# Kernel optimization log

Measured on AMD Instinct MI355X. Metric: run time of the kernel, lower is better.

The kernel has to match this reference:

```python
import jax, jax.numpy as jnp
import numpy as np

CODEBOOK_SIZE = 1024
EMBEDDING_DIM = 256
COMMITMENT_COST = 0.25


def setup_inputs() -> dict:
    key = jax.random.key(0)
    k1, k2 = jax.random.split(key)
    x = jax.random.normal(k1, (32, EMBEDDING_DIM, 32, 32), dtype=jnp.float32)
    # embedding initialized uniform(-1/K, 1/K) like the torch module
    embedding = jax.random.uniform(
        k2, (CODEBOOK_SIZE, EMBEDDING_DIM), dtype=jnp.float32,
        minval=-1.0 / CODEBOOK_SIZE, maxval=1.0 / CODEBOOK_SIZE)
    return {"x": x, "embedding": embedding}


def reference(x, embedding):
    # x: [B, C, H, W] -> inputs: [B, H, W, C]
    inputs = jnp.transpose(x, (0, 2, 3, 1))
    input_shape = inputs.shape
    flat = inputs.reshape(-1, EMBEDDING_DIM)  # [N, D]
    # squared L2 distances to codebook: [N, K]
    distances = (jnp.sum(flat ** 2, axis=1, keepdims=True)
                 + jnp.sum(embedding ** 2, axis=1)
                 - 2.0 * flat @ embedding.T)
    encoding_indices = jnp.argmin(distances, axis=1)  # [N]
    encodings = jax.nn.one_hot(encoding_indices, CODEBOOK_SIZE, dtype=jnp.float32)  # [N, K]
    # gather (same math as encodings @ embedding)
    quantized = embedding[encoding_indices].reshape(input_shape)  # [B, H, W, C]
    e_latent_loss = jnp.mean((jax.lax.stop_gradient(quantized) - inputs) ** 2)
    q_latent_loss = jnp.mean((quantized - jax.lax.stop_gradient(inputs)) ** 2)
    loss = q_latent_loss + COMMITMENT_COST * e_latent_loss
    # straight-through estimator
    quantized_st = inputs + jax.lax.stop_gradient(quantized - inputs)
    return (loss, jnp.transpose(quantized_st, (0, 3, 1, 2)), encodings)
```

## Files before the change

### kernel.cpp

```cpp
#include <hip/hip_runtime.h>
#include <cstdint>
#include <cstddef>

constexpr int B = 32, C = 256, H = 32, W = 32;
constexpr int NPTS = B * H * W;
constexpr int DIM  = 256;
constexpr int K    = 1024;
constexpr int QELEMS = B * C * H * W;
constexpr int CHW = C * H * W;

typedef __attribute__((ext_vector_type(8))) short s8v;
typedef __attribute__((ext_vector_type(4))) float f32x4;

#define GLD_LDS16(g, l)                                                        \
  __builtin_amdgcn_global_load_lds(                                            \
      (const __attribute__((address_space(1))) unsigned int*)(g),              \
      (__attribute__((address_space(3))) unsigned int*)(l), 16, 0, 0)

__device__ __forceinline__ unsigned short f2bf(float f) {
  unsigned u = __float_as_uint(f);
  return (unsigned short)((u + 0x7FFFu + ((u >> 16) & 1u)) >> 16);
}

__global__ __launch_bounds__(256) void prep_kernel(
    const float* __restrict__ x, const float* __restrict__ emb,
    unsigned short* __restrict__ ehi, float* __restrict__ esq,
    unsigned short* __restrict__ xhi, float* __restrict__ xsq) {
  __shared__ float xls[DIM][32];
  const int t = threadIdx.x;
  const int bid = blockIdx.x;

  if (bid < 16) {
    float (*sums)[64] = (float (*)[64])xls;
    const int k = bid * 64 + (t & 63);
    const int seg = t >> 6;
    const float* er = emb + (size_t)k * DIM + seg * 64;
    float v[64];
    float4* v4 = (float4*)v;
#pragma unroll
    for (int i = 0; i < 16; ++i) v4[i] = *(const float4*)(er + i * 4);
    float s = 0.f;
#pragma unroll
    for (int i = 0; i < 64; ++i) s = fmaf(v[i], v[i], s);
    unsigned short* eo = ehi + (size_t)k * DIM + seg * 64;
#pragma unroll
    for (int i = 0; i < 8; ++i) {
      unsigned short h[8];
#pragma unroll
      for (int j = 0; j < 8; ++j) h[j] = f2bf(v[i * 8 + j]);
      *(s8v*)(eo + i * 8) = *(s8v*)h;
    }
    sums[seg][t & 63] = s;
    __syncthreads();
    if (t < 64)
      esq[bid * 64 + t] =
          ((sums[0][t] + sums[1][t]) + sums[2][t]) + sums[3][t];
    return;
  }

  const int n0 = (bid - 16) * 32;
  const int bb = n0 >> 10, hw0 = n0 & 1023;
  const float* xb = x + (size_t)bb * CHW + hw0;
  const int lane = t & 63, w = t >> 6;
  const int row_off = lane >> 3;
  const int p4 = (lane & 7) * 4;
#pragma unroll
  for (int i = 0; i < 8; ++i) {
    const int c0 = w * 64 + i * 8;
    GLD_LDS16(xb + (size_t)(c0 + row_off) * 1024 + p4, &xls[c0][0]);
  }
  __syncthreads();

  if (t < 32) {
    float s = 0.f;
#pragma unroll 8
    for (int c = 0; c < 256; ++c) {
      const float v = xls[c][t];
      s = fmaf(v, v, s);
    }
    xsq[n0 + t] = s;
  }
  const int p2 = t & 31, cb = (t >> 5) * 32;
  unsigned short* xo = xhi + (size_t)(n0 + p2) * DIM + cb;
#pragma unroll
  for (int i = 0; i < 4; ++i) {
    unsigned short h[8];
#pragma unroll
    for (int j = 0; j < 8; ++j) h[j] = f2bf(xls[cb + i * 8 + j][p2]);
    *(s8v*)(xo + i * 8) = *(s8v*)h;
  }
}

constexpr float MARGIN = 1e-3f;
__global__ __launch_bounds__(256) void coarse_kernel(
    const unsigned short* __restrict__ xhi, const unsigned short* __restrict__ ehi,
    const float* __restrict__ esq, const float* __restrict__ xsq,
    float* __restrict__ part, unsigned int* __restrict__ cand) {
  __shared__ __align__(16) unsigned short xs[128][32];
  __shared__ __align__(16) unsigned short es[128][32];
  __shared__ float xsq_s[128], esq_s[128], thr_s[128];
  __shared__ unsigned long long red2[2][128];
  __shared__ unsigned int cntL[128];

  const int t = threadIdx.x;
  const int lane = t & 63, w = t >> 6;
  const int wn = (w & 1) * 64, wk = (w >> 1) * 64;
  const int col = lane & 15, quad = lane >> 4;
  const int nblk = blockIdx.x * 128;
  const int kblk = blockIdx.y * 128;

  if (t < 128) {
    xsq_s[t] = xsq[nblk + t];
    esq_s[t] = esq[kblk + t];
    cntL[t] = 0u;
  }

  f32x4 acc[4][4];
#pragma unroll
  for (int i = 0; i < 4; ++i)
#pragma unroll
    for (int j = 0; j < 4; ++j) acc[i][j] = (f32x4){0.f, 0.f, 0.f, 0.f};

  const int gl_row = lane >> 2;
  const int gl_c   = (lane & 3) * 8;

  for (int c0 = 0; c0 < DIM; c0 += 32) {
    __syncthreads();
#pragma unroll
    for (int i = 0; i < 2; ++i) {
      const int inst = w + 4 * i;
      const int row = inst * 16 + gl_row;
      GLD_LDS16(xhi + (size_t)(nblk + row) * DIM + c0 + gl_c, &xs[inst * 16][0]);
      GLD_LDS16(ehi + (size_t)(kblk + row) * DIM + c0 + gl_c, &es[inst * 16][0]);
    }
    __syncthreads();
    s8v a[4], b[4];
#pragma unroll
    for (int ti = 0; ti < 4; ++ti)
      a[ti] = *(const s8v*)&xs[wn + ti * 16 + col][quad * 8];
#pragma unroll
    for (int tj = 0; tj < 4; ++tj)
      b[tj] = *(const s8v*)&es[wk + tj * 16 + col][quad * 8];
#pragma unroll
    for (int ti = 0; ti < 4; ++ti)
#pragma unroll
      for (int tj = 0; tj < 4; ++tj)
        acc[ti][tj] = __builtin_amdgcn_mfma_f32_16x16x32_bf16(
            a[ti], b[tj], acc[ti][tj], 0, 0, 0);
  }

  unsigned long long nmin[4][4];
#pragma unroll
  for (int ti = 0; ti < 4; ++ti)
#pragma unroll
    for (int r = 0; r < 4; ++r) nmin[ti][r] = ~0ULL;
#pragma unroll
  for (int ti = 0; ti < 4; ++ti)
#pragma unroll
    for (int tj = 0; tj < 4; ++tj) {
      const int krel = wk + tj * 16 + col;
      const float eq = esq_s[krel];
#pragma unroll
      for (int r = 0; r < 4; ++r) {
        const int nl = wn + ti * 16 + quad * 4 + r;
        const float d = (xsq_s[nl] + eq) - 2.f * acc[ti][tj][r];
        const unsigned long long key =
            ((unsigned long long)__float_as_uint(d) << 32) |
            (unsigned)(kblk + krel);
        if (key < nmin[ti][r]) nmin[ti][r] = key;
      }
    }
#pragma unroll
  for (int o = 1; o < 16; o <<= 1)
#pragma unroll
    for (int ti = 0; ti < 4; ++ti)
#pragma unroll
      for (int r = 0; r < 4; ++r) {
        const unsigned long long v = __shfl_xor(nmin[ti][r], o, 64);
        if (v < nmin[ti][r]) nmin[ti][r] = v;
      }
  if (col == 0) {
#pragma unroll
    for (int ti = 0; ti < 4; ++ti)
#pragma unroll
      for (int r = 0; r < 4; ++r)
        red2[w >> 1][wn + ti * 16 + quad * 4 + r] = nmin[ti][r];
  }
  __syncthreads();
  if (t < 128) {
    const unsigned long long m0 = red2[0][t], m1 = red2[1][t];
    const unsigned long long m = (m1 < m0) ? m1 : m0;
    const float dmin = __uint_as_float((unsigned)(m >> 32));
    part[(size_t)(nblk + t) * 8 + blockIdx.y] = dmin;
    thr_s[t] = dmin + MARGIN;
  }
  __syncthreads();
#pragma unroll
  for (int ti = 0; ti < 4; ++ti)
#pragma unroll
    for (int tj = 0; tj < 4; ++tj) {
      const int krel = wk + tj * 16 + col;
      const float eq = esq_s[krel];
#pragma unroll
      for (int r = 0; r < 4; ++r) {
        const int nl = wn + ti * 16 + quad * 4 + r;
        const float d = (xsq_s[nl] + eq) - 2.f * acc[ti][tj][r];
        if (d <= thr_s[nl]) {
          const unsigned slot = atomicAdd(&cntL[nl], 1u);
          if (slot < 4u)
            cand[((size_t)(nblk + nl) * 8 + blockIdx.y) * 4 + slot] =
                (unsigned)(kblk + krel);
        }
      }
    }
  __syncthreads();
  if (t < 128) {
    unsigned c = cntL[t];
    const size_t base = ((size_t)(nblk + t) * 8 + blockIdx.y) * 4;
    if (c > 4u) { cand[base + 3] = 0xFFFFFFFEu; c = 3u; }
    for (unsigned s = c; s < 4u; ++s) cand[base + s] = 0xFFFFFFFFu;
  }
}

__global__ __launch_bounds__(256) void resolve_kernel(
    const float* __restrict__ x, const float* __restrict__ emb,
    const float* __restrict__ esq, const float* __restrict__ xsq,
    const float* __restrict__ part, const unsigned int* __restrict__ cand,
    int* __restrict__ ids_g) {
  __shared__ __align__(16) float xls[DIM][17];
  __shared__ unsigned list[512];
  __shared__ unsigned long long best[16];
  __shared__ float thr_s[16];
  __shared__ float xsq_s[16];
  __shared__ int lcnt;

  const int t = threadIdx.x;
  const int n0 = blockIdx.x * 16;
  const int bb = n0 >> 10, hw0 = n0 & 1023;

  const float* xb = x + (size_t)bb * CHW + hw0;
  {
    const int p = t & 15, cs = t >> 4;
#pragma unroll 4
    for (int r = 0; r < 16; ++r) {
      const int c = r * 16 + cs;
      xls[c][p] = xb[(size_t)c * 1024 + p];
    }
  }
  if (t == 0) lcnt = 0;
  if (t < 16) {
    best[t] = ~0ULL;
    xsq_s[t] = xsq[n0 + t];
    const float4 p0 = *(const float4*)&part[(size_t)(n0 + t) * 8];
    const float4 p1 = *(const float4*)&part[(size_t)(n0 + t) * 8 + 4];
    float g = fminf(fminf(fminf(p0.x, p0.y), fminf(p0.z, p0.w)),
                    fminf(fminf(p1.x, p1.y), fminf(p1.z, p1.w)));
    thr_s[t] = g + MARGIN;
  }
  __syncthreads();

  if (t < 128) {
    const int nn = t >> 3, s = t & 7;
    const float pv = part[(size_t)(n0 + nn) * 8 + s];
    if (pv <= thr_s[nn]) {
      const uint4 c4 = *(const uint4*)&cand[((size_t)(n0 + nn) * 8 + s) * 4];
      const unsigned vs[4] = {c4.x, c4.y, c4.z, c4.w};
#pragma unroll
      for (int i = 0; i < 4; ++i) {
        const unsigned v = vs[i];
        if (v == 0xFFFFFFFFu) continue;
        const unsigned entry = (v == 0xFFFFFFFEu)
                                   ? ((unsigned)nn << 11) | 1024u | (unsigned)s
                                   : ((unsigned)nn << 11) | (v & 1023u);
        const int pos = atomicAdd(&lcnt, 1);
        if (pos < 512) list[pos] = entry;
      }
    }
  }
  __syncthreads();

  const int L = lcnt < 512 ? lcnt : 512;
  for (int e = t; e < L; e += 256) {
    const unsigned entry = list[e];
    const int p = entry >> 11;
    const float xq = xsq_s[p];
    int klo, khi;
    if (entry & 1024u) { const int s = entry & 7; klo = s * 128; khi = klo + 128; }
    else               { klo = entry & 1023u; khi = klo + 1; }
    for (int k = klo; k < khi; ++k) {
      const float* er = emb + (size_t)k * DIM;
      float dot = 0.f;
#pragma unroll 4
      for (int c4 = 0; c4 < DIM; c4 += 4) {
        const float4 e4 = *(const float4*)(er + c4);
        dot = fmaf(xls[c4 + 0][p], e4.x, dot);
        dot = fmaf(xls[c4 + 1][p], e4.y, dot);
        dot = fmaf(xls[c4 + 2][p], e4.z, dot);
        dot = fmaf(xls[c4 + 3][p], e4.w, dot);
      }
      const float t1 = xq + esq[k];
      const float d = t1 - 2.f * dot;
      const unsigned long long key =
          ((unsigned long long)__float_as_uint(d) << 32) | (unsigned)k;
      atomicMin(&best[p], key);
    }
  }
  __syncthreads();
  if (t < 16) ids_g[n0 + t] = (int)(best[t] & 0xFFFFFFFFu);
}

__global__ __launch_bounds__(256) void enc_kernel(
    const int* __restrict__ ids_g, float* __restrict__ enc) {
  __shared__ int ids_s[16];
  const int t = threadIdx.x;
  const int n0 = blockIdx.x * 16;
  if (t < 16) ids_s[t] = ids_g[n0 + t];
  __syncthreads();

  float* sl = enc + (size_t)blockIdx.x * 16384;
  float4* b4 = (float4*)(sl + 3);
#pragma unroll
  for (int j = 0; j < 16; ++j) {
    const int idx = t + j * 256;
    if (idx < 4095) {
      const int lf = 3 + 4 * idx;
      float4 v;
      v.x = (((lf + 0) & 1023) == ids_s[(lf + 0) >> 10]) ? 1.f : 0.f;
      v.y = (((lf + 1) & 1023) == ids_s[(lf + 1) >> 10]) ? 1.f : 0.f;
      v.z = (((lf + 2) & 1023) == ids_s[(lf + 2) >> 10]) ? 1.f : 0.f;
      v.w = (((lf + 3) & 1023) == ids_s[(lf + 3) >> 10]) ? 1.f : 0.f;
      b4[idx] = v;
    }
  }
  if (t == 0) {
    sl[0] = (ids_s[0] == 0) ? 1.f : 0.f;
    sl[1] = (ids_s[0] == 1) ? 1.f : 0.f;
    sl[2] = (ids_s[0] == 2) ? 1.f : 0.f;
    sl[16383] = (ids_s[15] == 1023) ? 1.f : 0.f;
  }
}

__global__ __launch_bounds__(256) void outq_kernel(
    const float* __restrict__ x, const float* __restrict__ emb,
    const int* __restrict__ ids_g, float* __restrict__ outq,
    float* __restrict__ lws) {
  __shared__ int ids_s[1024];
  __shared__ float lred[4];
  const int t = threadIdx.x;
  const int bb = blockIdx.x >> 5;
  const int c0 = (blockIdx.x & 31) * 8;

#pragma unroll
  for (int i = 0; i < 4; ++i) ids_s[t + i * 256] = ids_g[bb * 1024 + t + i * 256];
  __syncthreads();

  const float* xb = x + (size_t)bb * CHW;
  float* ob = outq + (size_t)bb * CHW;
  float lsum = 0.f;
#pragma unroll
  for (int i = 0; i < 4; ++i) {
    const int hw = t + i * 256;
    const int id = ids_s[hw];
    const float* er = emb + (size_t)id * DIM + c0;
    const float4 e0 = *(const float4*)(er);
    const float4 e1 = *(const float4*)(er + 4);
    const float q[8] = {e0.x, e0.y, e0.z, e0.w, e1.x, e1.y, e1.z, e1.w};
#pragma unroll
    for (int ci = 0; ci < 8; ++ci) {
      const float xv = xb[(size_t)(c0 + ci) * 1024 + hw];
      ob[(size_t)(c0 + ci) * 1024 + hw] = q[ci];
      const float d = q[ci] - xv;
      lsum = fmaf(d, d, lsum);
    }
  }

  float s = lsum;
#pragma unroll
  for (int o = 32; o > 0; o >>= 1) s += __shfl_down(s, o, 64);
  if ((t & 63) == 0) lred[t >> 6] = s;
  __syncthreads();
  if (t == 0)
    lws[blockIdx.x] = ((lred[0] + lred[1]) + lred[2]) + lred[3];
}

__global__ __launch_bounds__(256) void loss_reduce(
    const float* __restrict__ lws, float* __restrict__ loss) {
  __shared__ float red[4];
  const int t = threadIdx.x;
  float s = 0.f;
#pragma unroll
  for (int i = 0; i < 4; ++i) s += lws[t + i * 256];
#pragma unroll
  for (int o = 32; o > 0; o >>= 1) s += __shfl_down(s, o, 64);
  if ((t & 63) == 0) red[t >> 6] = s;
  __syncthreads();
  if (t == 0)
    *loss = (((red[0] + red[1]) + red[2]) + red[3]) * (1.25f / (float)QELEMS);
}

extern "C" void kernel_launch(void* const* d_in, const int* in_sizes, int n_in,
                              void* d_out, int out_size, void* d_ws, size_t ws_size,
                              hipStream_t stream) {
  const float* x   = (const float*)d_in[0];
  const float* emb = (const float*)d_in[1];
  float* out  = (float*)d_out;
  float* loss = out;
  float* outq = out + 1;
  float* enc  = out + 1 + QELEMS;

  char* ws = (char*)d_ws;
  unsigned short* ehi  = (unsigned short*)ws;
  float*          esq  = (float*)(ws + 524288);
  float*          xsq  = (float*)(ws + 528384);
  float*          part = (float*)(ws + 659456);
  unsigned int*   cand = (unsigned int*)(ws + 1708032);
  unsigned short* xhi  = (unsigned short*)(ws + 5902336);
  float*          lws  = (float*)(ws + 22679552);
  int*            ids  = (int*)(ws + 22683648);

  prep_kernel<<<16 + 1024, 256, 0, stream>>>(x, emb, ehi, esq, xhi, xsq);
  dim3 cg(NPTS / 128, 8);
  coarse_kernel<<<cg, 256, 0, stream>>>(xhi, ehi, esq, xsq, part, cand);
  resolve_kernel<<<NPTS / 16, 256, 0, stream>>>(x, emb, esq, xsq, part, cand,
                                                ids);
  enc_kernel<<<NPTS / 16, 256, 0, stream>>>(ids, enc);
  outq_kernel<<<1024, 256, 0, stream>>>(x, emb, ids, outq, lws);
  loss_reduce<<<1, 256, 0, stream>>>(lws, loss);
}
```

Baseline: 293.2 us.

## Fuse one-hot and quantized output kernels and derive loss from min distances

The resolve kernel now handles 32 points per block and computes each block's loss partial by summing the winning squared distances. This removes the need to re-read x in a separate loss pass. The one-hot encoding writer and the quantized-output gather are merged into one kernel, and both use nontemporal stores. The aim is to save the extra full read of x plus one kernel launch, at the cost of computing the loss from the expanded-distance formula, which can lose some precision to cancellation.

```diff
diff --git a/kernel.cpp b/kernel.cpp
--- a/kernel.cpp
+++ b/kernel.cpp
@@ -20,6 +20,13 @@
 __device__ __forceinline__ unsigned short f2bf(float f) {
   unsigned u = __float_as_uint(f);
   return (unsigned short)((u + 0x7FFFu + ((u >> 16) & 1u)) >> 16);
+}
+
+__device__ __forceinline__ void nt_store4(float* p, f32x4 v) {
+  __builtin_nontemporal_store(v, (f32x4*)p);
+}
+__device__ __forceinline__ void nt_store1(float* p, float v) {
+  __builtin_nontemporal_store(v, p);
 }
 
 __global__ __launch_bounds__(256) void prep_kernel(
@@ -226,29 +233,29 @@
     const float* __restrict__ x, const float* __restrict__ emb,
     const float* __restrict__ esq, const float* __restrict__ xsq,
     const float* __restrict__ part, const unsigned int* __restrict__ cand,
-    int* __restrict__ ids_g) {
-  __shared__ __align__(16) float xls[DIM][17];
-  __shared__ unsigned list[512];
-  __shared__ unsigned long long best[16];
-  __shared__ float thr_s[16];
-  __shared__ float xsq_s[16];
+    int* __restrict__ ids_g, float* __restrict__ lws) {
+  __shared__ __align__(16) float xls[DIM][33];
+  __shared__ unsigned list[1024];
+  __shared__ unsigned long long best[32];
+  __shared__ float thr_s[32];
+  __shared__ float xsq_s[32];
   __shared__ int lcnt;
 
   const int t = threadIdx.x;
-  const int n0 = blockIdx.x * 16;
+  const int n0 = blockIdx.x * 32;
   const int bb = n0 >> 10, hw0 = n0 & 1023;
 
   const float* xb = x + (size_t)bb * CHW + hw0;
   {
-    const int p = t & 15, cs = t >> 4;
-#pragma unroll 4
-    for (int r = 0; r < 16; ++r) {
-      const int c = r * 16 + cs;
+    const int p = t & 31, cs = t >> 5;
+#pragma unroll 8
+    for (int r = 0; r < 32; ++r) {
+      const int c = r * 8 + cs;
       xls[c][p] = xb[(size_t)c * 1024 + p];
     }
   }
   if (t == 0) lcnt = 0;
-  if (t < 16) {
+  if (t < 32) {
     best[t] = ~0ULL;
     xsq_s[t] = xsq[n0 + t];
     const float4 p0 = *(const float4*)&part[(size_t)(n0 + t) * 8];
@@ -259,7 +266,7 @@
   }
   __syncthreads();
 
-  if (t < 128) {
+  {
     const int nn = t >> 3, s = t & 7;
     const float pv = part[(size_t)(n0 + nn) * 8 + s];
     if (pv <= thr_s[nn]) {
@@ -273,13 +280,13 @@
                                    ? ((unsigned)nn << 11) | 1024u | (unsigned)s
                                    : ((unsigned)nn << 11) | (v & 1023u);
         const int pos = atomicAdd(&lcnt, 1);
-        if (pos < 512) list[pos] = entry;
-      }
-    }
-  }
-  __syncthreads();
-
-  const int L = lcnt < 512 ? lcnt : 512;
+        if (pos < 1024) list[pos] = entry;
+      }
+    }
+  }
+  __syncthreads();
+
+  const int L = lcnt < 1024 ? lcnt : 1024;
   for (int e = t; e < L; e += 256) {
     const unsigned entry = list[e];
     const int p = entry >> 11;
@@ -306,81 +313,64 @@
     }
   }
   __syncthreads();
-  if (t < 16) ids_g[n0 + t] = (int)(best[t] & 0xFFFFFFFFu);
-}
-
-__global__ __launch_bounds__(256) void enc_kernel(
-    const int* __restrict__ ids_g, float* __restrict__ enc) {
-  __shared__ int ids_s[16];
+  if (t < 32) {
+    ids_g[n0 + t] = (int)(best[t] & 0xFFFFFFFFu);
+    float s = __uint_as_float((unsigned)(best[t] >> 32));
+#pragma unroll
+    for (int o = 16; o > 0; o >>= 1) s += __shfl_down(s, o, 64);
+    if (t == 0) lws[blockIdx.x] = s;
+  }
+}
+
+__global__ __launch_bounds__(256) void encq_kernel(
+    const float* __restrict__ emb, const int* __restrict__ ids_g,
+    float* __restrict__ enc, float* __restrict__ outq) {
+  __shared__ int ids_s[32];
   const int t = threadIdx.x;
-  const int n0 = blockIdx.x * 16;
-  if (t < 16) ids_s[t] = ids_g[n0 + t];
-  __syncthreads();
-
-  float* sl = enc + (size_t)blockIdx.x * 16384;
-  float4* b4 = (float4*)(sl + 3);
-#pragma unroll
-  for (int j = 0; j < 16; ++j) {
-    const int idx = t + j * 256;
-    if (idx < 4095) {
-      const int lf = 3 + 4 * idx;
-      float4 v;
-      v.x = (((lf + 0) & 1023) == ids_s[(lf + 0) >> 10]) ? 1.f : 0.f;
-      v.y = (((lf + 1) & 1023) == ids_s[(lf + 1) >> 10]) ? 1.f : 0.f;
-      v.z = (((lf + 2) & 1023) == ids_s[(lf + 2) >> 10]) ? 1.f : 0.f;
-      v.w = (((lf + 3) & 1023) == ids_s[(lf + 3) >> 10]) ? 1.f : 0.f;
-      b4[idx] = v;
-    }
-  }
-  if (t == 0) {
-    sl[0] = (ids_s[0] == 0) ? 1.f : 0.f;
-    sl[1] = (ids_s[0] == 1) ? 1.f : 0.f;
-    sl[2] = (ids_s[0] == 2) ? 1.f : 0.f;
-    sl[16383] = (ids_s[15] == 1023) ? 1.f : 0.f;
-  }
-}
-
-__global__ __launch_bounds__(256) void outq_kernel(
-    const float* __restrict__ x, const float* __restrict__ emb,
-    const int* __restrict__ ids_g, float* __restrict__ outq,
-    float* __restrict__ lws) {
-  __shared__ int ids_s[1024];
-  __shared__ float lred[4];
-  const int t = threadIdx.x;
-  const int bb = blockIdx.x >> 5;
-  const int c0 = (blockIdx.x & 31) * 8;
-
-#pragma unroll
-  for (int i = 0; i < 4; ++i) ids_s[t + i * 256] = ids_g[bb * 1024 + t + i * 256];
-  __syncthreads();
-
-  const float* xb = x + (size_t)bb * CHW;
-  float* ob = outq + (size_t)bb * CHW;
-  float lsum = 0.f;
-#pragma unroll
-  for (int i = 0; i < 4; ++i) {
-    const int hw = t + i * 256;
-    const int id = ids_s[hw];
-    const float* er = emb + (size_t)id * DIM + c0;
-    const float4 e0 = *(const float4*)(er);
-    const float4 e1 = *(const float4*)(er + 4);
-    const float q[8] = {e0.x, e0.y, e0.z, e0.w, e1.x, e1.y, e1.z, e1.w};
-#pragma unroll
-    for (int ci = 0; ci < 8; ++ci) {
-      const float xv = xb[(size_t)(c0 + ci) * 1024 + hw];
-      ob[(size_t)(c0 + ci) * 1024 + hw] = q[ci];
-      const float d = q[ci] - xv;
-      lsum = fmaf(d, d, lsum);
-    }
-  }
-
-  float s = lsum;
-#pragma unroll
-  for (int o = 32; o > 0; o >>= 1) s += __shfl_down(s, o, 64);
-  if ((t & 63) == 0) lred[t >> 6] = s;
-  __syncthreads();
-  if (t == 0)
-    lws[blockIdx.x] = ((lred[0] + lred[1]) + lred[2]) + lred[3];
+  const int n0 = blockIdx.x * 32;
+  const int bb = n0 >> 10, hw0 = n0 & 1023;
+  if (t < 32) ids_s[t] = ids_g[n0 + t];
+  __syncthreads();
+
+  float* sl = enc + (size_t)n0 * K;
+  {
+    float* b4 = sl + 3;
+#pragma unroll
+    for (int j = 0; j < 32; ++j) {
+      const int idx = t + j * 256;
+      if (idx < 8191) {
+        const int lf = 3 + 4 * idx;
+        f32x4 v;
+        v.x = (((lf + 0) & 1023) == ids_s[(lf + 0) >> 10]) ? 1.f : 0.f;
+        v.y = (((lf + 1) & 1023) == ids_s[(lf + 1) >> 10]) ? 1.f : 0.f;
+        v.z = (((lf + 2) & 1023) == ids_s[(lf + 2) >> 10]) ? 1.f : 0.f;
+        v.w = (((lf + 3) & 1023) == ids_s[(lf + 3) >> 10]) ? 1.f : 0.f;
+        nt_store4(b4 + 4 * idx, v);
+      }
+    }
+    if (t == 0) {
+      nt_store1(sl + 0, (ids_s[0] == 0) ? 1.f : 0.f);
+      nt_store1(sl + 1, (ids_s[0] == 1) ? 1.f : 0.f);
+      nt_store1(sl + 2, (ids_s[0] == 2) ? 1.f : 0.f);
+      nt_store1(sl + 32767, (ids_s[31] == 1023) ? 1.f : 0.f);
+    }
+  }
+
+  {
+    const int p = t & 31, g = t >> 5;
+    const int row = ids_s[p];
+    const float* er = emb + (size_t)row * DIM + g * 32;
+    float* ob = outq + (size_t)bb * CHW + hw0 + p;
+#pragma unroll
+    for (int i = 0; i < 8; ++i) {
+      const float4 v = *(const float4*)(er + i * 4);
+      const int c = g * 32 + i * 4;
+      nt_store1(ob + (size_t)(c + 0) * 1024, v.x);
+      nt_store1(ob + (size_t)(c + 1) * 1024, v.y);
+      nt_store1(ob + (size_t)(c + 2) * 1024, v.z);
+      nt_store1(ob + (size_t)(c + 3) * 1024, v.w);
+    }
+  }
 }
 
 __global__ __launch_bounds__(256) void loss_reduce(
@@ -421,9 +411,8 @@
   prep_kernel<<<16 + 1024, 256, 0, stream>>>(x, emb, ehi, esq, xhi, xsq);
   dim3 cg(NPTS / 128, 8);
   coarse_kernel<<<cg, 256, 0, stream>>>(xhi, ehi, esq, xsq, part, cand);
-  resolve_kernel<<<NPTS / 16, 256, 0, stream>>>(x, emb, esq, xsq, part, cand,
-                                                ids);
-  enc_kernel<<<NPTS / 16, 256, 0, stream>>>(ids, enc);
-  outq_kernel<<<1024, 256, 0, stream>>>(x, emb, ids, outq, lws);
+  resolve_kernel<<<NPTS / 32, 256, 0, stream>>>(x, emb, esq, xsq, part, cand,
+                                                ids, lws);
+  encq_kernel<<<NPTS / 32, 256, 0, stream>>>(emb, ids, enc, outq);
   loss_reduce<<<1, 256, 0, stream>>>(lws, loss);
 }
```

Result: slower. 302.8 us (+3.3%).
